# Performance work log

Measured on AMD Instinct MI355X. Metric: run time of the kernel, lower is better.

The kernel has to match this reference:

```python
import jax, jax.numpy as jnp
import numpy as np

HIDDEN = 1024
HEADS = 16
HEAD_DIM = HIDDEN // HEADS


def setup_inputs() -> dict:
    key = jax.random.key(0)
    ks = jax.random.split(key, 7)
    B, S = 4, 2048
    xav = float(np.sqrt(6.0 / (HIDDEN + HIDDEN)))  # xavier uniform bound
    def lin(k):
        return jax.random.uniform(k, (HIDDEN, HIDDEN), jnp.float32, -xav, xav)
    return {
        "hidden_states": jax.random.normal(ks[0], (B, S, HIDDEN), jnp.float32),
        "Wq": lin(ks[1]), "bq": jnp.zeros((HIDDEN,), jnp.float32),
        "Wk": lin(ks[2]), "bk": jnp.zeros((HIDDEN,), jnp.float32),
        "Wv": lin(ks[3]), "bv": jnp.zeros((HIDDEN,), jnp.float32),
    }


def reference(hidden_states, Wq, bq, Wk, bk, Wv, bv):
    B, S, H = hidden_states.shape
    def split_heads(t):  # [B,S,H] -> [B,heads,S,head_dim]
        return t.reshape(B, S, HEADS, HEAD_DIM).transpose(0, 2, 1, 3)
    q = split_heads(hidden_states @ Wq + bq)
    k = split_heads(hidden_states @ Wk + bk)
    v = split_heads(hidden_states @ Wv + bv)
    scores = jnp.einsum("bhqd,bhkd->bhqk", q, k) / jnp.sqrt(
        jnp.asarray(HEAD_DIM, hidden_states.dtype))
    probs = jax.nn.softmax(scores, axis=-1)  # dropout p=0.0 (inference)
    ctx = jnp.einsum("bhqk,bhkd->bhqd", probs, v)
    ctx = ctx.transpose(0, 2, 1, 3).reshape(B, S, H)
    return ctx
```

## Files before the change

### kernel.cpp

```cpp
#include <hip/hip_runtime.h>
#include <hip/hip_bf16.h>
#include <cstdint>

#define HIDDEN 1024
#define HEADS 16
#define HDIM 64
#define BATCH 4
#define SEQ 2048
#define MTOT (BATCH * SEQ)

typedef __attribute__((ext_vector_type(8))) short bfrag;
typedef __attribute__((ext_vector_type(4))) float cfrag;
typedef __attribute__((ext_vector_type(4))) float float4v;
typedef __attribute__((ext_vector_type(4))) unsigned short ushort4v;
typedef __attribute__((ext_vector_type(2))) unsigned int uint2v;

#define AS1 __attribute__((address_space(1)))
#define AS3 __attribute__((address_space(3)))

__device__ __forceinline__ void gl_lds16(const void* g, void* l) {
  __builtin_amdgcn_global_load_lds((AS1 void*)g, (AS3 void*)l, 16, 0, 0);
}

__device__ __forceinline__ uint16_t f2b(float f) {
  union { float f; uint32_t u; } v; v.f = f;
  uint32_t u = v.u;
  return (uint16_t)((u + 0x7FFFu + ((u >> 16) & 1u)) >> 16);
}

__global__ __launch_bounds__(256) void cvt_kernel(
    const float* __restrict__ x, const float* __restrict__ W0,
    const float* __restrict__ W1, const float* __restrict__ W2,
    uint16_t* __restrict__ Xb, uint16_t* __restrict__ Wt) {
  int bid = blockIdx.x;
  if (bid < 4096) {
    int i = bid * 256 + threadIdx.x;
    float4v a = ((const float4v*)x)[2 * i];
    float4v b = ((const float4v*)x)[2 * i + 1];
    bfrag o;
    o[0] = (short)f2b(a[0]); o[1] = (short)f2b(a[1]);
    o[2] = (short)f2b(a[2]); o[3] = (short)f2b(a[3]);
    o[4] = (short)f2b(b[0]); o[5] = (short)f2b(b[1]);
    o[6] = (short)f2b(b[2]); o[7] = (short)f2b(b[3]);
    ((bfrag*)Xb)[i] = o;
    return;
  }
  int id = bid - 4096;
  int z = id >> 8, rem = id & 255;
  const float* W = z == 0 ? W0 : (z == 1 ? W1 : W2);
  uint16_t* out = Wt + (size_t)z * HIDDEN * HIDDEN;
  __shared__ float tile[64][65];
  int n0 = (rem & 15) * 64, k0 = (rem >> 4) * 64;
  int t = threadIdx.x;
  int r = t >> 2, cq = (t & 3) * 16;
#pragma unroll
  for (int i = 0; i < 16; i += 4) {
    float4v v = *(const float4v*)&W[(size_t)(k0 + r) * HIDDEN + n0 + cq + i];
    tile[r][cq + i + 0] = v[0]; tile[r][cq + i + 1] = v[1];
    tile[r][cq + i + 2] = v[2]; tile[r][cq + i + 3] = v[3];
  }
  __syncthreads();
  bfrag o0, o1;
#pragma unroll
  for (int i = 0; i < 8; ++i) o0[i] = (short)f2b(tile[cq + i][r]);
#pragma unroll
  for (int i = 0; i < 8; ++i) o1[i] = (short)f2b(tile[cq + 8 + i][r]);
  *(bfrag*)&out[(size_t)(n0 + r) * HIDDEN + k0 + cq] = o0;
  *(bfrag*)&out[(size_t)(n0 + r) * HIDDEN + k0 + cq + 8] = o1;
}

__global__ __launch_bounds__(256) void gemm_qkv_kernel(
    const uint16_t* __restrict__ X, const uint16_t* __restrict__ Wt,
    const float* __restrict__ b0, const float* __restrict__ b1,
    const float* __restrict__ b2,
    uint16_t* __restrict__ Qo, uint16_t* __restrict__ Ko, uint16_t* __restrict__ Vo) {
  __shared__ uint16_t As[128 * 32];
  __shared__ uint16_t Bs[128 * 32];
  int which = blockIdx.z;
  const uint16_t* Wp = Wt + (size_t)which * HIDDEN * HIDDEN;
  const float* bias = which == 0 ? b0 : (which == 1 ? b1 : b2);

  int m0 = blockIdx.x * 128, n0 = blockIdx.y * 128;
  int tid = threadIdx.x;
  int wave = tid >> 6, lane = tid & 63;
  int wm = wave >> 1, wn = wave & 1;
  int g = lane >> 4, c = lane & 15;
  int sr = lane >> 2;
  int sc = (lane & 3) * 8;

  cfrag acc[4][4];
#pragma unroll
  for (int i = 0; i < 4; ++i)
#pragma unroll
    for (int jj = 0; jj < 4; ++jj) acc[i][jj] = cfrag{0.f, 0.f, 0.f, 0.f};

  for (int kt = 0; kt < HIDDEN / 32; ++kt) {
    int kc = kt * 32 + sc;
#pragma unroll
    for (int i = 0; i < 2; ++i) {
      int rowA = (i * 4 + wave) * 16;
      gl_lds16(&X[(size_t)(m0 + rowA + sr) * HIDDEN + kc], &As[rowA * 32]);
      gl_lds16(&Wp[(size_t)(n0 + rowA + sr) * HIDDEN + kc], &Bs[rowA * 32]);
    }
    __syncthreads();
    bfrag af[4], bf[4];
#pragma unroll
    for (int mt = 0; mt < 4; ++mt)
      af[mt] = *(const bfrag*)&As[(wm * 64 + mt * 16 + c) * 32 + g * 8];
#pragma unroll
    for (int nt = 0; nt < 4; ++nt)
      bf[nt] = *(const bfrag*)&Bs[(wn * 64 + nt * 16 + c) * 32 + g * 8];
#pragma unroll
    for (int mt = 0; mt < 4; ++mt)
#pragma unroll
      for (int nt = 0; nt < 4; ++nt)
        acc[mt][nt] = __builtin_amdgcn_mfma_f32_16x16x32_bf16(af[mt], bf[nt],
                                                              acc[mt][nt], 0, 0, 0);
    __syncthreads();
  }

  if (which == 2) {
    int bb_ = m0 >> 11;
    int s0 = (m0 & 2047) + wm * 64;
#pragma unroll
    for (int nt = 0; nt < 4; ++nt) {
      int n = n0 + wn * 64 + nt * 16 + c;
      int h = n >> 6, d = n & 63;
      float bb = bias[n];
      size_t base = ((size_t)(bb_ * 16 + h) * 64 + d) * SEQ;
#pragma unroll
      for (int mt = 0; mt < 4; ++mt) {
        int s = s0 + mt * 16 + g * 4;
        ushort4v pk;
        pk[0] = f2b(acc[mt][nt][0] + bb);
        pk[1] = f2b(acc[mt][nt][1] + bb);
        pk[2] = f2b(acc[mt][nt][2] + bb);
        pk[3] = f2b(acc[mt][nt][3] + bb);
        *(ushort4v*)&Vo[base + s] = pk;
      }
    }
  } else {
    uint16_t* out = which == 0 ? Qo : Ko;
    float sc_ = which == 0 ? 0.125f * 1.44269504088896f : 1.0f;
#pragma unroll
    for (int nt = 0; nt < 4; ++nt) {
      int n = n0 + wn * 64 + nt * 16 + c;
      float bb = bias[n];
#pragma unroll
      for (int mt = 0; mt < 4; ++mt) {
        int mb = m0 + wm * 64 + mt * 16 + g * 4;
#pragma unroll
        for (int r = 0; r < 4; ++r)
          out[(size_t)(mb + r) * HIDDEN + n] = f2b((acc[mt][nt][r] + bb) * sc_);
      }
    }
  }
}

__global__ __launch_bounds__(256, 3) void attn_kernel(
    const uint16_t* __restrict__ Q, const uint16_t* __restrict__ K,
    const uint16_t* __restrict__ VT, float* __restrict__ out) {
  __shared__ uint16_t Ks[2][64 * 64];
  __shared__ uint16_t Vs[2][64 * 64];
  __shared__ __align__(16) uint16_t Pl[4][32][64];

  int bid = blockIdx.x;
  int wg = (bid & 7) * 128 + (bid >> 3);
  int bh = wg >> 4, qt = wg & 15;
  int b = bh >> 4, h = bh & 15;
  int tid = threadIdx.x, wave = tid >> 6, lane = tid & 63;
  int g = lane >> 4, c = lane & 15;
  size_t rowb = (size_t)b * SEQ;
  int colb = h * HDIM;
  const uint16_t* Kh = K + rowb * HIDDEN + colb;
  const uint16_t* Vh = VT + (size_t)bh * HDIM * SEQ;

  int r8 = lane >> 3, c8 = lane & 7;
  int scol = ((c8 ^ r8) << 3);
  int sbrow = (wave & 1) * 32;

  int qrow = qt * 128 + wave * 32 + c;
  bfrag aq0[2], aq1[2];
#pragma unroll
  for (int kb = 0; kb < 2; ++kb) {
    aq0[kb] = *(const bfrag*)&Q[(rowb + qrow) * HIDDEN + colb + kb * 32 + g * 8];
    aq1[kb] = *(const bfrag*)&Q[(rowb + qrow + 16) * HIDDEN + colb + kb * 32 + g * 8];
  }

  float mr0 = -INFINITY, lr0 = 0.f;
  float mr1 = -INFINITY, lr1 = 0.f;
  cfrag oacc0[4], oacc1[4];
#pragma unroll
  for (int dt = 0; dt < 4; ++dt) {
    oacc0[dt] = cfrag{0.f, 0.f, 0.f, 0.f};
    oacc1[dt] = cfrag{0.f, 0.f, 0.f, 0.f};
  }

  if (wave < 2) {
#pragma unroll
    for (int j = 0; j < 4; ++j) {
      int rl = sbrow + j * 8;
      gl_lds16(&Kh[(size_t)(rl + r8) * HIDDEN + scol], &Ks[0][rl * 64]);
    }
  } else {
#pragma unroll
    for (int j = 0; j < 4; ++j) {
      int rl = sbrow + j * 8;
      gl_lds16(&Vh[(size_t)(rl + r8) * SEQ + scol], &Vs[0][rl * 64]);
    }
  }
  __syncthreads();

  int cur = 0;
  int sw = (c & 7) << 4;
  uint8_t* Pb0 = (uint8_t*)Pl + wave * 4096 + c * 128;
  uint8_t* Pb1 = Pb0 + 16 * 128;

  for (int t = 0; t < 32; ++t) {
    int j0 = t * 64;
    if (t < 31) {
      int jn = j0 + 64;
      if (wave < 2) {
#pragma unroll
        for (int j = 0; j < 4; ++j) {
          int rl = sbrow + j * 8;
          gl_lds16(&Kh[(size_t)(jn + rl + r8) * HIDDEN + scol],
                   &Ks[cur ^ 1][rl * 64]);
        }
      } else {
#pragma unroll
        for (int j = 0; j < 4; ++j) {
          int rl = sbrow + j * 8;
          gl_lds16(&Vh[(size_t)(rl + r8) * SEQ + jn + scol],
                   &Vs[cur ^ 1][rl * 64]);
        }
      }
    }

    const uint8_t* Kbuf = (const uint8_t*)Ks[cur];
    const uint8_t* Vbuf = (const uint8_t*)Vs[cur];

    cfrag s0[4], s1[4];
#pragma unroll
    for (int nt = 0; nt < 4; ++nt) {
      s0[nt] = cfrag{0.f, 0.f, 0.f, 0.f};
      s1[nt] = cfrag{0.f, 0.f, 0.f, 0.f};
    }
    __builtin_amdgcn_s_setprio(1);
#pragma unroll
    for (int kb = 0; kb < 2; ++kb) {
#pragma unroll
      for (int nt = 0; nt < 4; ++nt) {
        int off = ((nt * 16 + c) * 128 + kb * 64 + g * 16) ^ sw;
        bfrag bk = *(const bfrag*)(Kbuf + off);
        s0[nt] = __builtin_amdgcn_mfma_f32_16x16x32_bf16(bk, aq0[kb], s0[nt], 0, 0, 0);
        s1[nt] = __builtin_amdgcn_mfma_f32_16x16x32_bf16(bk, aq1[kb], s1[nt], 0, 0, 0);
      }
    }
    __builtin_amdgcn_s_setprio(0);

    {
      float mx = fmaxf(fmaxf(s0[0][0], s0[0][1]), s0[0][2]);
      mx = fmaxf(fmaxf(mx, s0[0][3]), s0[1][0]);
      mx = fmaxf(fmaxf(mx, s0[1][1]), s0[1][2]);
      mx = fmaxf(fmaxf(mx, s0[1][3]), s0[2][0]);
      mx = fmaxf(fmaxf(mx, s0[2][1]), s0[2][2]);
      mx = fmaxf(fmaxf(mx, s0[2][3]), s0[3][0]);
      mx = fmaxf(fmaxf(mx, s0[3][1]), s0[3][2]);
      mx = fmaxf(mx, s0[3][3]);
      mx = fmaxf(mx, __shfl_xor(mx, 16, 64));
      mx = fmaxf(mx, __shfl_xor(mx, 32, 64));
      if (mx > mr0 + 8.0f) {
        float alpha = __builtin_amdgcn_exp2f(mr0 - mx);
        lr0 *= alpha;
#pragma unroll
        for (int dt = 0; dt < 4; ++dt)
#pragma unroll
          for (int r = 0; r < 4; ++r) oacc0[dt][r] *= alpha;
        mr0 = mx;
      }
      float ps = 0.f;
#pragma unroll
      for (int nt = 0; nt < 4; ++nt) {
#pragma unroll
        for (int r = 0; r < 4; ++r)
          s0[nt][r] = __builtin_amdgcn_exp2f(s0[nt][r] - mr0);
        ps += (s0[nt][0] + s0[nt][1]) + (s0[nt][2] + s0[nt][3]);
      }
      lr0 += ps;
#pragma unroll
      for (int nt = 0; nt < 4; ++nt) {
        uint32_t w0, w1;
        asm("v_cvt_pk_bf16_f32 %0, %1, %2" : "=v"(w0) : "v"(s0[nt][0]), "v"(s0[nt][1]));
        asm("v_cvt_pk_bf16_f32 %0, %1, %2" : "=v"(w1) : "v"(s0[nt][2]), "v"(s0[nt][3]));
        uint2v pw; pw[0] = w0; pw[1] = w1;
        *(uint2v*)(Pb0 + ((nt * 32 + g * 8) ^ sw)) = pw;
      }
    }
    {
      float mx = fmaxf(fmaxf(s1[0][0], s1[0][1]), s1[0][2]);
      mx = fmaxf(fmaxf(mx, s1[0][3]), s1[1][0]);
      mx = fmaxf(fmaxf(mx, s1[1][1]), s1[1][2]);
      mx = fmaxf(fmaxf(mx, s1[1][3]), s1[2][0]);
      mx = fmaxf(fmaxf(mx, s1[2][1]), s1[2][2]);
      mx = fmaxf(fmaxf(mx, s1[2][3]), s1[3][0]);
      mx = fmaxf(fmaxf(mx, s1[3][1]), s1[3][2]);
      mx = fmaxf(mx, s1[3][3]);
      mx = fmaxf(mx, __shfl_xor(mx, 16, 64));
      mx = fmaxf(mx, __shfl_xor(mx, 32, 64));
      if (mx > mr1 + 8.0f) {
        float alpha = __builtin_amdgcn_exp2f(mr1 - mx);
        lr1 *= alpha;
#pragma unroll
        for (int dt = 0; dt < 4; ++dt)
#pragma unroll
          for (int r = 0; r < 4; ++r) oacc1[dt][r] *= alpha;
        mr1 = mx;
      }
      float ps = 0.f;
#pragma unroll
      for (int nt = 0; nt < 4; ++nt) {
#pragma unroll
        for (int r = 0; r < 4; ++r)
          s1[nt][r] = __builtin_amdgcn_exp2f(s1[nt][r] - mr1);
        ps += (s1[nt][0] + s1[nt][1]) + (s1[nt][2] + s1[nt][3]);
      }
      lr1 += ps;
#pragma unroll
      for (int nt = 0; nt < 4; ++nt) {
        uint32_t w0, w1;
        asm("v_cvt_pk_bf16_f32 %0, %1, %2" : "=v"(w0) : "v"(s1[nt][0]), "v"(s1[nt][1]));
        asm("v_cvt_pk_bf16_f32 %0, %1, %2" : "=v"(w1) : "v"(s1[nt][2]), "v"(s1[nt][3]));
        uint2v pw; pw[0] = w0; pw[1] = w1;
        *(uint2v*)(Pb1 + ((nt * 32 + g * 8) ^ sw)) = pw;
      }
    }

    __builtin_amdgcn_s_setprio(1);
#pragma unroll
    for (int kb = 0; kb < 2; ++kb) {
      bfrag ap0 = *(const bfrag*)(Pb0 + ((kb * 64 + g * 16) ^ sw));
      bfrag ap1 = *(const bfrag*)(Pb1 + ((kb * 64 + g * 16) ^ sw));
#pragma unroll
      for (int dt = 0; dt < 4; ++dt) {
        int off = ((dt * 16 + c) * 128 + kb * 64 + g * 16) ^ sw;
        bfrag bv = *(const bfrag*)(Vbuf + off);
        oacc0[dt] = __builtin_amdgcn_mfma_f32_16x16x32_bf16(bv, ap0, oacc0[dt], 0, 0, 0);
        oacc1[dt] = __builtin_amdgcn_mfma_f32_16x16x32_bf16(bv, ap1, oacc1[dt], 0, 0, 0);
      }
    }
    __builtin_amdgcn_s_setprio(0);

    __syncthreads();
    cur ^= 1;
  }

  lr0 += __shfl_xor(lr0, 16, 64);
  lr0 += __shfl_xor(lr0, 32, 64);
  lr1 += __shfl_xor(lr1, 16, 64);
  lr1 += __shfl_xor(lr1, 32, 64);
  float inv0 = 1.0f / lr0, inv1 = 1.0f / lr1;
  size_t orow = rowb + (size_t)qt * 128 + wave * 32 + c;
#pragma unroll
  for (int dt = 0; dt < 4; ++dt) {
    float4v o;
    o[0] = oacc0[dt][0] * inv0; o[1] = oacc0[dt][1] * inv0;
    o[2] = oacc0[dt][2] * inv0; o[3] = oacc0[dt][3] * inv0;
    *(float4v*)&out[orow * HIDDEN + colb + dt * 16 + g * 4] = o;
    float4v p;
    p[0] = oacc1[dt][0] * inv1; p[1] = oacc1[dt][1] * inv1;
    p[2] = oacc1[dt][2] * inv1; p[3] = oacc1[dt][3] * inv1;
    *(float4v*)&out[(orow + 16) * HIDDEN + colb + dt * 16 + g * 4] = p;
  }
}

extern "C" void kernel_launch(void* const* d_in, const int* in_sizes, int n_in,
                              void* d_out, int out_size, void* d_ws, size_t ws_size,
                              hipStream_t stream) {
  const float* x  = (const float*)d_in[0];
  const float* Wq = (const float*)d_in[1];
  const float* bq = (const float*)d_in[2];
  const float* Wk = (const float*)d_in[3];
  const float* bk = (const float*)d_in[4];
  const float* Wv = (const float*)d_in[5];
  const float* bv = (const float*)d_in[6];
  float* out = (float*)d_out;

  uint8_t* ws = (uint8_t*)d_ws;
  const size_t XB = 0;
  const size_t WT = XB + (size_t)MTOT * HIDDEN * 2;
  const size_t QB = WT + (size_t)3 * HIDDEN * HIDDEN * 2;
  const size_t KB = QB + (size_t)MTOT * HIDDEN * 2;
  const size_t VB = KB + (size_t)MTOT * HIDDEN * 2;
  uint16_t* Xb = (uint16_t*)(ws + XB);
  uint16_t* Wt = (uint16_t*)(ws + WT);
  uint16_t* Qb = (uint16_t*)(ws + QB);
  uint16_t* Kb = (uint16_t*)(ws + KB);
  uint16_t* Vb = (uint16_t*)(ws + VB);

  cvt_kernel<<<dim3(4096 + 768), 256, 0, stream>>>(x, Wq, Wk, Wv, Xb, Wt);
  gemm_qkv_kernel<<<dim3(64, 8, 3), 256, 0, stream>>>(Xb, Wt, bq, bk, bv, Qb, Kb, Vb);
  attn_kernel<<<dim3(1024), 256, 0, stream>>>(Qb, Kb, Vb, out);
}
```

Baseline: 272.9 us.

## Fuse Q/K/V projections into one GEMM block sharing the X tile

The QKV GEMM now computes all three projections in a single block, loading the X tile once and reusing it against three weight tiles instead of launching a separate z-slice per projection. This removes two-thirds of the X tile loads and cuts the grid from 1536 to 512 blocks. The cost is three times the accumulator registers (48 cfrags per thread), with launch bounds set to 2 and s_setprio around the MFMA section. Fewer blocks and higher register pressure may reduce occupancy and leave the 256 CUs less well filled.

```diff
diff --git a/kernel.cpp b/kernel.cpp
--- a/kernel.cpp
+++ b/kernel.cpp
@@ -69,16 +69,13 @@
   *(bfrag*)&out[(size_t)(n0 + r) * HIDDEN + k0 + cq + 8] = o1;
 }
 
-__global__ __launch_bounds__(256) void gemm_qkv_kernel(
+__global__ __launch_bounds__(256, 2) void gemm_qkv_kernel(
     const uint16_t* __restrict__ X, const uint16_t* __restrict__ Wt,
     const float* __restrict__ b0, const float* __restrict__ b1,
     const float* __restrict__ b2,
     uint16_t* __restrict__ Qo, uint16_t* __restrict__ Ko, uint16_t* __restrict__ Vo) {
   __shared__ uint16_t As[128 * 32];
-  __shared__ uint16_t Bs[128 * 32];
-  int which = blockIdx.z;
-  const uint16_t* Wp = Wt + (size_t)which * HIDDEN * HIDDEN;
-  const float* bias = which == 0 ? b0 : (which == 1 ? b1 : b2);
+  __shared__ uint16_t Bs[3][128 * 32];
 
   int m0 = blockIdx.x * 128, n0 = blockIdx.y * 128;
   int tid = threadIdx.x;
@@ -88,11 +85,15 @@
   int sr = lane >> 2;
   int sc = (lane & 3) * 8;
 
-  cfrag acc[4][4];
+  cfrag accQ[4][4], accK[4][4], accV[4][4];
 #pragma unroll
   for (int i = 0; i < 4; ++i)
 #pragma unroll
-    for (int jj = 0; jj < 4; ++jj) acc[i][jj] = cfrag{0.f, 0.f, 0.f, 0.f};
+    for (int j = 0; j < 4; ++j) {
+      accQ[i][j] = cfrag{0.f, 0.f, 0.f, 0.f};
+      accK[i][j] = cfrag{0.f, 0.f, 0.f, 0.f};
+      accV[i][j] = cfrag{0.f, 0.f, 0.f, 0.f};
+    }
 
   for (int kt = 0; kt < HIDDEN / 32; ++kt) {
     int kc = kt * 32 + sc;
@@ -100,58 +101,106 @@
     for (int i = 0; i < 2; ++i) {
       int rowA = (i * 4 + wave) * 16;
       gl_lds16(&X[(size_t)(m0 + rowA + sr) * HIDDEN + kc], &As[rowA * 32]);
-      gl_lds16(&Wp[(size_t)(n0 + rowA + sr) * HIDDEN + kc], &Bs[rowA * 32]);
+      gl_lds16(&Wt[(size_t)(n0 + rowA + sr) * HIDDEN + kc],
+               &Bs[0][rowA * 32]);
+      gl_lds16(&Wt[(size_t)HIDDEN * HIDDEN + (size_t)(n0 + rowA + sr) * HIDDEN + kc],
+               &Bs[1][rowA * 32]);
+      gl_lds16(&Wt[(size_t)2 * HIDDEN * HIDDEN + (size_t)(n0 + rowA + sr) * HIDDEN + kc],
+               &Bs[2][rowA * 32]);
     }
     __syncthreads();
-    bfrag af[4], bf[4];
+    bfrag af[4];
 #pragma unroll
     for (int mt = 0; mt < 4; ++mt)
       af[mt] = *(const bfrag*)&As[(wm * 64 + mt * 16 + c) * 32 + g * 8];
-#pragma unroll
-    for (int nt = 0; nt < 4; ++nt)
-      bf[nt] = *(const bfrag*)&Bs[(wn * 64 + nt * 16 + c) * 32 + g * 8];
-#pragma unroll
-    for (int mt = 0; mt < 4; ++mt)
+    __builtin_amdgcn_s_setprio(1);
+    {
+      bfrag bf[4];
 #pragma unroll
       for (int nt = 0; nt < 4; ++nt)
-        acc[mt][nt] = __builtin_amdgcn_mfma_f32_16x16x32_bf16(af[mt], bf[nt],
-                                                              acc[mt][nt], 0, 0, 0);
+        bf[nt] = *(const bfrag*)&Bs[0][(wn * 64 + nt * 16 + c) * 32 + g * 8];
+#pragma unroll
+      for (int mt = 0; mt < 4; ++mt)
+#pragma unroll
+        for (int nt = 0; nt < 4; ++nt)
+          accQ[mt][nt] = __builtin_amdgcn_mfma_f32_16x16x32_bf16(af[mt], bf[nt],
+                                                                 accQ[mt][nt], 0, 0, 0);
+    }
+    {
+      bfrag bf[4];
+#pragma unroll
+      for (int nt = 0; nt < 4; ++nt)
+        bf[nt] = *(const bfrag*)&Bs[1][(wn * 64 + nt * 16 + c) * 32 + g * 8];
+#pragma unroll
+      for (int mt = 0; mt < 4; ++mt)
+#pragma unroll
+        for (int nt = 0; nt < 4; ++nt)
+          accK[mt][nt] = __builtin_amdgcn_mfma_f32_16x16x32_bf16(af[mt], bf[nt],
+                                                                 accK[mt][nt], 0, 0, 0);
+    }
+    {
+      bfrag bf[4];
+#pragma unroll
+      for (int nt = 0; nt < 4; ++nt)
+        bf[nt] = *(const bfrag*)&Bs[2][(wn * 64 + nt * 16 + c) * 32 + g * 8];
+#pragma unroll
+      for (int mt = 0; mt < 4; ++mt)
+#pragma unroll
+        for (int nt = 0; nt < 4; ++nt)
+          accV[mt][nt] = __builtin_amdgcn_mfma_f32_16x16x32_bf16(af[mt], bf[nt],
+                                                                 accV[mt][nt], 0, 0, 0);
+    }
+    __builtin_amdgcn_s_setprio(0);
     __syncthreads();
   }
 
-  if (which == 2) {
+  {
+    const float sc_ = 0.125f * 1.44269504088896f;
+#pragma unroll
+    for (int nt = 0; nt < 4; ++nt) {
+      int n = n0 + wn * 64 + nt * 16 + c;
+      float bb = b0[n];
+#pragma unroll
+      for (int mt = 0; mt < 4; ++mt) {
+        int mb = m0 + wm * 64 + mt * 16 + g * 4;
+#pragma unroll
+        for (int r = 0; r < 4; ++r)
+          Qo[(size_t)(mb + r) * HIDDEN + n] = f2b((accQ[mt][nt][r] + bb) * sc_);
+      }
+    }
+  }
+  {
+#pragma unroll
+    for (int nt = 0; nt < 4; ++nt) {
+      int n = n0 + wn * 64 + nt * 16 + c;
+      float bb = b1[n];
+#pragma unroll
+      for (int mt = 0; mt < 4; ++mt) {
+        int mb = m0 + wm * 64 + mt * 16 + g * 4;
+#pragma unroll
+        for (int r = 0; r < 4; ++r)
+          Ko[(size_t)(mb + r) * HIDDEN + n] = f2b(accK[mt][nt][r] + bb);
+      }
+    }
+  }
+  {
     int bb_ = m0 >> 11;
     int s0 = (m0 & 2047) + wm * 64;
 #pragma unroll
     for (int nt = 0; nt < 4; ++nt) {
       int n = n0 + wn * 64 + nt * 16 + c;
       int h = n >> 6, d = n & 63;
-      float bb = bias[n];
+      float bb = b2[n];
       size_t base = ((size_t)(bb_ * 16 + h) * 64 + d) * SEQ;
 #pragma unroll
       for (int mt = 0; mt < 4; ++mt) {
         int s = s0 + mt * 16 + g * 4;
         ushort4v pk;
-        pk[0] = f2b(acc[mt][nt][0] + bb);
-        pk[1] = f2b(acc[mt][nt][1] + bb);
-        pk[2] = f2b(acc[mt][nt][2] + bb);
-        pk[3] = f2b(acc[mt][nt][3] + bb);
+        pk[0] = f2b(accV[mt][nt][0] + bb);
+        pk[1] = f2b(accV[mt][nt][1] + bb);
+        pk[2] = f2b(accV[mt][nt][2] + bb);
+        pk[3] = f2b(accV[mt][nt][3] + bb);
         *(ushort4v*)&Vo[base + s] = pk;
-      }
-    }
-  } else {
-    uint16_t* out = which == 0 ? Qo : Ko;
-    float sc_ = which == 0 ? 0.125f * 1.44269504088896f : 1.0f;
-#pragma unroll
-    for (int nt = 0; nt < 4; ++nt) {
-      int n = n0 + wn * 64 + nt * 16 + c;
-      float bb = bias[n];
-#pragma unroll
-      for (int mt = 0; mt < 4; ++mt) {
-        int mb = m0 + wm * 64 + mt * 16 + g * 4;
-#pragma unroll
-        for (int r = 0; r < 4; ++r)
-          out[(size_t)(mb + r) * HIDDEN + n] = f2b((acc[mt][nt][r] + bb) * sc_);
       }
     }
   }
@@ -399,6 +448,6 @@
   uint16_t* Vb = (uint16_t*)(ws + VB);
 
   cvt_kernel<<<dim3(4096 + 768), 256, 0, stream>>>(x, Wq, Wk, Wv, Xb, Wt);
-  gemm_qkv_kernel<<<dim3(64, 8, 3), 256, 0, stream>>>(Xb, Wt, bq, bk, bv, Qb, Kb, Vb);
+  gemm_qkv_kernel<<<dim3(64, 8), 256, 0, stream>>>(Xb, Wt, bq, bk, bv, Qb, Kb, Vb);
   attn_kernel<<<dim3(1024), 256, 0, stream>>>(Qb, Kb, Vb, out);
 }
```

Result: faster. 258.2 us (-5.4%).
